# Performance work log

Measured on AMD Instinct MI355X. Metric: run time of the kernel, lower is better.

## Reference

```python
import jax, jax.numpy as jnp
import numpy as np

IMG = 128          # image_size
TEX = 4            # texture_size (hard-coded in module)
WIDTH = float(np.tan(np.radians(30.0)))  # nr default viewing_angle=30
NEAR = 0.1
# images dict: values are [distance, azimuth, elevation]; eye = get_points_from_angles(dist, elev, azim)
VIEWS = [(2.83, 45.0, 0.0), (2.0, 0.0, 90.0), (3.46, 45.0, 45.0), (3.0, 0.0, 0.0)]  # (dist, elev, azim)


def _eye_from_angles(dist, elev_deg, azim_deg):
    e, a = np.radians(elev_deg), np.radians(azim_deg)
    return jnp.asarray([dist * np.cos(e) * np.sin(a), dist * np.sin(e), -dist * np.cos(e) * np.cos(a)], jnp.float32)


def _normalize(v):
    return v / jnp.linalg.norm(v)


def _trilinear(tex, c):
    # tex: [P, T, T, T, 3], c: [P, 3] continuous coords in [0, T-1]
    i0 = jnp.clip(jnp.floor(c).astype(jnp.int32), 0, TEX - 2)
    f = c - i0.astype(c.dtype)
    pi = jnp.arange(tex.shape[0])
    out = jnp.zeros((tex.shape[0], 3), tex.dtype)
    for dx in (0, 1):
        for dy in (0, 1):
            for dz in (0, 1):
                wgt = ((f[:, 0] if dx else 1.0 - f[:, 0])
                       * (f[:, 1] if dy else 1.0 - f[:, 1])
                       * (f[:, 2] if dz else 1.0 - f[:, 2]))
                out = out + wgt[:, None] * tex[pi, i0[:, 0] + dx, i0[:, 1] + dy, i0[:, 2] + dz]
    return out


def _render(verts, faces, tex, eye):
    # verts [V,3], faces [F,3] int, tex [F,T,T,T,3] -> image [1,3,IMG,IMG]
    # look_at transform (at=origin, up=+y)
    z_ax = _normalize(-eye)
    x_ax = _normalize(jnp.cross(jnp.asarray([0.0, 1.0, 0.0], jnp.float32), z_ax))
    y_ax = _normalize(jnp.cross(z_ax, x_ax))
    R = jnp.stack([x_ax, y_ax, z_ax])                       # [3,3]
    v = (verts - eye) @ R.T                                 # [V,3]
    # perspective projection
    z = v[:, 2]
    v = jnp.stack([v[:, 0] / (z * WIDTH), v[:, 1] / (z * WIDTH), z], -1)
    fv = v[faces]                                           # [F,3,3]

    # pixel grid in NDC [-1,1], row 0 = top
    s = (jnp.arange(IMG, dtype=jnp.float32) + 0.5) / IMG * 2.0 - 1.0
    px = jnp.broadcast_to(s[None, :], (IMG, IMG)).ravel()
    py = jnp.broadcast_to(-s[:, None], (IMG, IMG)).ravel()
    p = jnp.stack([px, py], -1)                             # [P,2]

    v0 = fv[:, 0, :2]
    e1 = fv[:, 1, :2] - v0
    e2 = fv[:, 2, :2] - v0
    det = e1[:, 0] * e2[:, 1] - e1[:, 1] * e2[:, 0]         # [F]
    ok = jnp.abs(det) > 1e-8
    inv_det = jnp.where(ok, 1.0 / jnp.where(ok, det, 1.0), 0.0)
    d = p[None, :, :] - v0[:, None, :]                      # [F,P,2]
    w1 = (e2[:, None, 1] * d[..., 0] - e2[:, None, 0] * d[..., 1]) * inv_det[:, None]
    w2 = (-e1[:, None, 1] * d[..., 0] + e1[:, None, 0] * d[..., 1]) * inv_det[:, None]
    w0 = 1.0 - w1 - w2
    fz = fv[:, :, 2]                                        # [F,3]
    depth = w0 * fz[:, 0:1] + w1 * fz[:, 1:2] + w2 * fz[:, 2:3]  # [F,P]
    visible = (w0 >= 0) & (w1 >= 0) & (w2 >= 0) & ok[:, None] & (depth > NEAR)
    depth_m = jnp.where(visible, depth, jnp.inf)
    fidx = jnp.argmin(depth_m, axis=0)                      # [P]
    P = fidx.shape[0]
    pi = jnp.arange(P)
    hit = jnp.isfinite(depth_m[fidx, pi])
    wsel = jnp.stack([w0[fidx, pi], w1[fidx, pi], w2[fidx, pi]], -1)  # [P,3]
    coords = jnp.clip(wsel, 0.0, 1.0) * (TEX - 1)
    color = _trilinear(tex[fidx], coords) * hit[:, None].astype(tex.dtype)  # [P,3]
    return color.reshape(IMG, IMG, 3).transpose(2, 0, 1)[None]  # [1,3,IMG,IMG]


def setup_inputs() -> dict:
    key = jax.random.key(0)
    k1, k2, k3, k4 = jax.random.split(key, 4)
    V, F = 1024, 1024
    vertices = jax.random.normal(k1, (1, V, 3), jnp.float32) * 0.5
    faces = jax.random.randint(k2, (1, F, 3), 0, V, jnp.int32)
    textures = jax.random.normal(k3, (1, F, TEX, TEX, TEX, 3), jnp.float32)
    image_refs = jax.random.uniform(k4, (4, 1, IMG, IMG), jnp.float32)
    return {"vertices": vertices, "faces": faces, "textures": textures, "image_refs": image_refs}


def reference(vertices, faces, textures, image_refs):
    tex = jnp.tanh(textures)[0]   # [F,T,T,T,3]
    verts = vertices[0]
    fcs = faces[0]
    loss = jnp.float32(0.0)
    for c, (dist, elev, azim) in enumerate(VIEWS):
        image = _render(verts, fcs, tex, _eye_from_angles(dist, elev, azim))  # [1,3,H,W]
        ref = image_refs[c][:, None]                                          # [1,1,H,W]
        loss = loss + jnp.sum((image - ref) ** 2)
    return loss
```

## Files before the change

### kernel.cpp

```cpp
#include <hip/hip_runtime.h>
#include <math.h>

#define IMG 128
#define NPIX (IMG * IMG)
#define NF 1024
#define NCHUNK 8
#define CHF (NF / NCHUNK)
#define FSTRIDE 12
#define NEAR_Z 0.1f

struct AllViews { float m[4][12]; };

__global__ void precompute_faces(const float* __restrict__ verts,
                                 const int* __restrict__ faces,
                                 float* __restrict__ fd,
                                 AllViews vc, float W)
{
    int t = blockIdx.x * blockDim.x + threadIdx.x;
    if (t >= 4 * NF) return;
    int view = t >> 10, f = t & (NF - 1);
    const float* M = vc.m[view];

    float proj[3][3];
    for (int k = 0; k < 3; ++k) {
        int vi = faces[f * 3 + k];
        float px = verts[vi * 3 + 0] - M[9];
        float py = verts[vi * 3 + 1] - M[10];
        float pz = verts[vi * 3 + 2] - M[11];
        float x = M[0] * px + M[1] * py + M[2] * pz;
        float y = M[3] * px + M[4] * py + M[5] * pz;
        float z = M[6] * px + M[7] * py + M[8] * pz;
        proj[k][0] = x / (z * W);
        proj[k][1] = y / (z * W);
        proj[k][2] = z;
    }
    float v0x = proj[0][0], v0y = proj[0][1];
    float e1x = proj[1][0] - v0x, e1y = proj[1][1] - v0y;
    float e2x = proj[2][0] - v0x, e2y = proj[2][1] - v0y;
    float det = e1x * e2y - e1y * e2x;
    bool ok = fabsf(det) > 1e-8f;
    float inv = ok ? 1.0f / det : 0.0f;

    float a1x = e2y * inv, a1y = -e2x * inv;
    float b1 = -(a1x * v0x + a1y * v0y);
    float a2x = -e1y * inv, a2y = e1x * inv;
    float b2 = -(a2x * v0x + a2y * v0y);
    float g1 = proj[1][2] - proj[0][2];
    float g2 = proj[2][2] - proj[0][2];
    float ddx = g1 * a1x + g2 * a2x;
    float ddy = g1 * a1y + g2 * a2y;
    float dc  = proj[0][2] + g1 * b1 + g2 * b2;
    if (!ok) dc = 0.0f;

    float* o = fd + (size_t)(view * NF + f) * FSTRIDE;
    o[0] = a1x; o[1] = a1y; o[2] = b1;  o[3] = a2x;
    o[4] = a2y; o[5] = b2;  o[6] = ddx; o[7] = ddy;
    o[8] = dc;  o[9] = 0.0f; o[10] = 0.0f; o[11] = 0.0f;
}

__global__ __launch_bounds__(256) void raster(
    const float* __restrict__ fd,
    unsigned long long* __restrict__ keys)
{
    __shared__ float4 lds4[CHF * 3];

    int bid = blockIdx.x;
    int view  = bid >> 9;
    int b     = bid & 511;
    int chunk = b & (NCHUNK - 1);
    int ptile = b >> 3;
    int tid = threadIdx.x;

    const float4* src = (const float4*)fd + (size_t)(view * NF + chunk * CHF) * 3;
    for (int i = tid; i < CHF * 3; i += 256) lds4[i] = src[i];
    __syncthreads();

    int p = ptile * 256 + tid;
    int row = p >> 7, col = p & 127;
    float sx = ((col + 0.5f) * (1.0f / IMG)) * 2.0f - 1.0f;
    float sy = -(((row + 0.5f) * (1.0f / IMG)) * 2.0f - 1.0f);

    float best = INFINITY;
    int bf = 0;
    const float* ldsf = (const float*)lds4;

#pragma unroll 4
    for (int f = 0; f < CHF; ++f) {
        float4 Q0 = lds4[f * 3 + 0];
        float4 Q1 = lds4[f * 3 + 1];
        float dc  = ldsf[f * 12 + 8];
        float w1 = fmaf(Q0.x, sx, fmaf(Q0.y, sy, Q0.z));
        float w2 = fmaf(Q0.w, sx, fmaf(Q1.x, sy, Q1.y));
        float dep = fmaf(Q1.z, sx, fmaf(Q1.w, sy, dc));
        float s = w1 + w2;
        bool vis = (fminf(w1, w2) >= 0.0f) && (s <= 1.0f) && (dep > NEAR_Z);
        bool take = vis && (dep < best);
        best = take ? dep : best;
        bf   = take ? f : bf;
    }

    unsigned int dbits = __float_as_uint(best);
    unsigned long long key =
        ((unsigned long long)dbits << 32) |
        (unsigned int)(view * 0 + chunk * CHF + bf);
    atomicMin(&keys[view * NPIX + p], key);
}

__global__ __launch_bounds__(256) void shade_loss(
    const float* __restrict__ fd,
    const unsigned long long* __restrict__ keys,
    const float* __restrict__ tex,
    const float* __restrict__ refs,
    float* __restrict__ out)
{
    __shared__ float wsum[4];
    int t = blockIdx.x * blockDim.x + threadIdx.x;
    int view = t >> 14, p = t & (NPIX - 1);
    int row = p >> 7, col = p & 127;
    float sx = ((col + 0.5f) * (1.0f / IMG)) * 2.0f - 1.0f;
    float sy = -(((row + 0.5f) * (1.0f / IMG)) * 2.0f - 1.0f);

    unsigned long long key = keys[view * NPIX + p];
    bool hit = (unsigned int)(key >> 32) < 0x7f800000u;
    float ref = refs[t];
    float lossv;
    if (hit) {
        int f = (int)(key & 0xffffffffu);
        const float4* Q = (const float4*)fd + (size_t)(view * NF + f) * 3;
        float4 Q0 = Q[0];
        float4 Q1 = Q[1];
        float w1 = fmaf(Q0.x, sx, fmaf(Q0.y, sy, Q0.z));
        float w2 = fmaf(Q0.w, sx, fmaf(Q1.x, sy, Q1.y));
        float w0 = 1.0f - w1 - w2;
        float cx = fminf(fmaxf(w0, 0.0f), 1.0f) * 3.0f;
        float cy = fminf(fmaxf(w1, 0.0f), 1.0f) * 3.0f;
        float cz = fminf(fmaxf(w2, 0.0f), 1.0f) * 3.0f;
        int ix = min(max((int)floorf(cx), 0), 2);
        int iy = min(max((int)floorf(cy), 0), 2);
        int iz = min(max((int)floorf(cz), 0), 2);
        float fx = cx - (float)ix, fy = cy - (float)iy, fz = cz - (float)iz;

        const float* T = tex + (size_t)f * 192;
        float c0 = 0.0f, c1 = 0.0f, c2 = 0.0f;
        for (int dxi = 0; dxi < 2; ++dxi)
            for (int dyi = 0; dyi < 2; ++dyi)
                for (int dzi = 0; dzi < 2; ++dzi) {
                    float w = (dxi ? fx : 1.0f - fx) *
                              (dyi ? fy : 1.0f - fy) *
                              (dzi ? fz : 1.0f - fz);
                    int base = (((ix + dxi) * 4 + (iy + dyi)) * 4 + (iz + dzi)) * 3;
                    c0 += w * tanhf(T[base + 0]);
                    c1 += w * tanhf(T[base + 1]);
                    c2 += w * tanhf(T[base + 2]);
                }
        float d0 = c0 - ref, d1 = c1 - ref, d2 = c2 - ref;
        lossv = d0 * d0 + d1 * d1 + d2 * d2;
    } else {
        lossv = 3.0f * ref * ref;
    }

    for (int off = 32; off; off >>= 1) lossv += __shfl_down(lossv, off);
    int tid = threadIdx.x;
    if ((tid & 63) == 0) wsum[tid >> 6] = lossv;
    __syncthreads();
    if (tid == 0) atomicAdd(out, wsum[0] + wsum[1] + wsum[2] + wsum[3]);
}

static void make_view(double dist, double elev, double azim, float* M)
{
    double e = elev * M_PI / 180.0, a = azim * M_PI / 180.0;
    float ex = (float)(dist * cos(e) * sin(a));
    float ey = (float)(dist * sin(e));
    float ez = (float)(-dist * cos(e) * cos(a));
    float zx = -ex, zy = -ey, zz = -ez;
    float n = sqrtf(zx * zx + zy * zy + zz * zz);
    zx /= n; zy /= n; zz /= n;
    float xx = zz, xy = 0.0f, xz = -zx;
    n = sqrtf(xx * xx + xy * xy + xz * xz);
    xx /= n; xy /= n; xz /= n;
    float yx = zy * xz - zz * xy;
    float yy = zz * xx - zx * xz;
    float yz = zx * xy - zy * xx;
    n = sqrtf(yx * yx + yy * yy + yz * yz);
    yx /= n; yy /= n; yz /= n;
    M[0] = xx; M[1] = xy; M[2] = xz;
    M[3] = yx; M[4] = yy; M[5] = yz;
    M[6] = zx; M[7] = zy; M[8] = zz;
    M[9] = ex; M[10] = ey; M[11] = ez;
}

extern "C" void kernel_launch(void* const* d_in, const int* in_sizes, int n_in,
                              void* d_out, int out_size, void* d_ws, size_t ws_size,
                              hipStream_t stream)
{
    const float* verts = (const float*)d_in[0];
    const int*   faces = (const int*)d_in[1];
    const float* tex   = (const float*)d_in[2];
    const float* refs  = (const float*)d_in[3];
    float* out = (float*)d_out;

    float* fd = (float*)d_ws;
    unsigned long long* keys =
        (unsigned long long*)((char*)d_ws + 4 * NF * FSTRIDE * sizeof(float));

    AllViews vc;
    const double V[4][3] = {{2.83, 45.0, 0.0}, {2.0, 0.0, 90.0},
                            {3.46, 45.0, 45.0}, {3.0, 0.0, 0.0}};
    for (int i = 0; i < 4; ++i) make_view(V[i][0], V[i][1], V[i][2], vc.m[i]);
    float W = (float)tan(M_PI / 6.0);

    hipMemsetAsync(out, 0, sizeof(float), stream);
    hipMemsetAsync(keys, 0xFF, 4 * NPIX * sizeof(unsigned long long), stream);
    precompute_faces<<<16, 256, 0, stream>>>(verts, faces, fd, vc, W);
    raster<<<2048, 256, 0, stream>>>(fd, keys);
    shade_loss<<<256, 256, 0, stream>>>(fd, keys, tex, refs, out);
}
```

Baseline: 49.65 us.

## Replace atomicMin depth keys with per-chunk buffers and deterministic final reduce

The raster kernel now writes one depth/face key per chunk per pixel instead of doing a 64-bit atomicMin, and the shade kernel takes the min over the 8 chunk keys. The float atomicAdd on the output is replaced by per-block partial sums plus a small one-block final reduction. Both memsets go away. The aim is to remove atomic traffic and memset launches, at the cost of 8x more key storage and reads plus one extra kernel launch.

```diff
diff --git a/kernel.cpp b/kernel.cpp
--- a/kernel.cpp
+++ b/kernel.cpp
@@ -8,6 +8,7 @@
 #define CHF (NF / NCHUNK)
 #define FSTRIDE 12
 #define NEAR_Z 0.1f
+#define NSHADE_BLK 256
 
 struct AllViews { float m[4][12]; };
 
@@ -102,8 +103,8 @@
     unsigned int dbits = __float_as_uint(best);
     unsigned long long key =
         ((unsigned long long)dbits << 32) |
-        (unsigned int)(view * 0 + chunk * CHF + bf);
-    atomicMin(&keys[view * NPIX + p], key);
+        (unsigned int)(chunk * CHF + bf);
+    keys[((size_t)(view * NCHUNK + chunk) << 14) + p] = key;
 }
 
 __global__ __launch_bounds__(256) void shade_loss(
@@ -111,7 +112,7 @@
     const unsigned long long* __restrict__ keys,
     const float* __restrict__ tex,
     const float* __restrict__ refs,
-    float* __restrict__ out)
+    float* __restrict__ partial)
 {
     __shared__ float wsum[4];
     int t = blockIdx.x * blockDim.x + threadIdx.x;
@@ -120,7 +121,14 @@
     float sx = ((col + 0.5f) * (1.0f / IMG)) * 2.0f - 1.0f;
     float sy = -(((row + 0.5f) * (1.0f / IMG)) * 2.0f - 1.0f);
 
-    unsigned long long key = keys[view * NPIX + p];
+    const unsigned long long* kb = keys + ((size_t)(view * NCHUNK) << 14) + p;
+    unsigned long long key = ~0ULL;
+#pragma unroll
+    for (int c = 0; c < NCHUNK; ++c) {
+        unsigned long long k = kb[(size_t)c << 14];
+        key = (k < key) ? k : key;
+    }
+
     bool hit = (unsigned int)(key >> 32) < 0x7f800000u;
     float ref = refs[t];
     float lossv;
@@ -163,7 +171,19 @@
     int tid = threadIdx.x;
     if ((tid & 63) == 0) wsum[tid >> 6] = lossv;
     __syncthreads();
-    if (tid == 0) atomicAdd(out, wsum[0] + wsum[1] + wsum[2] + wsum[3]);
+    if (tid == 0) partial[blockIdx.x] = wsum[0] + wsum[1] + wsum[2] + wsum[3];
+}
+
+__global__ __launch_bounds__(256) void final_reduce(
+    const float* __restrict__ partial, float* __restrict__ out)
+{
+    __shared__ float wsum[4];
+    int tid = threadIdx.x;
+    float v = partial[tid];
+    for (int off = 32; off; off >>= 1) v += __shfl_down(v, off);
+    if ((tid & 63) == 0) wsum[tid >> 6] = v;
+    __syncthreads();
+    if (tid == 0) out[0] = wsum[0] + wsum[1] + wsum[2] + wsum[3];
 }
 
 static void make_view(double dist, double elev, double azim, float* M)
@@ -199,9 +219,12 @@
     const float* refs  = (const float*)d_in[3];
     float* out = (float*)d_out;
 
-    float* fd = (float*)d_ws;
-    unsigned long long* keys =
-        (unsigned long long*)((char*)d_ws + 4 * NF * FSTRIDE * sizeof(float));
+    char* ws = (char*)d_ws;
+    float* fd = (float*)ws;
+    ws += 4 * NF * FSTRIDE * sizeof(float);
+    unsigned long long* keys = (unsigned long long*)ws;
+    ws += (size_t)4 * NCHUNK * NPIX * sizeof(unsigned long long);
+    float* partial = (float*)ws;
 
     AllViews vc;
     const double V[4][3] = {{2.83, 45.0, 0.0}, {2.0, 0.0, 90.0},
@@ -209,9 +232,8 @@
     for (int i = 0; i < 4; ++i) make_view(V[i][0], V[i][1], V[i][2], vc.m[i]);
     float W = (float)tan(M_PI / 6.0);
 
-    hipMemsetAsync(out, 0, sizeof(float), stream);
-    hipMemsetAsync(keys, 0xFF, 4 * NPIX * sizeof(unsigned long long), stream);
     precompute_faces<<<16, 256, 0, stream>>>(verts, faces, fd, vc, W);
     raster<<<2048, 256, 0, stream>>>(fd, keys);
-    shade_loss<<<256, 256, 0, stream>>>(fd, keys, tex, refs, out);
-}
+    shade_loss<<<NSHADE_BLK, 256, 0, stream>>>(fd, keys, tex, refs, partial);
+    final_reduce<<<1, 256, 0, stream>>>(partial, out);
+}
```

After: 45.94 us. 1.08x faster.
